# Optimization experiments

Hardware: AMD Instinct MI355X
Metric: run time of the kernel (lower is better)

The kernel has to match this reference:

```python
import jax, jax.numpy as jnp
import numpy as np

B, T, H = 32, 4096, 512


def setup_inputs() -> dict:
    key = jax.random.key(0)
    k1, k2, k3, k4, k5 = jax.random.split(key, 5)
    stdv = 1.0 / np.sqrt(2 * H)
    stdv_v = 1.0 / np.sqrt(H)
    return {
        "hidden": jax.random.normal(k1, (B, H), dtype=jnp.float32),
        "encoder_outputs": jax.random.normal(k2, (T, B, H), dtype=jnp.float32),
        "W_attn": jax.random.uniform(k3, (H, 2 * H), minval=-stdv, maxval=stdv, dtype=jnp.float32),
        "b_attn": jax.random.uniform(k4, (H,), minval=-stdv, maxval=stdv, dtype=jnp.float32),
        "v": jax.random.uniform(k5, (H,), minval=-stdv_v, maxval=stdv_v, dtype=jnp.float32),
    }


def reference(hidden, encoder_outputs, W_attn, b_attn, v):
    # hidden: [B, H]; encoder_outputs: [T, B, H]
    T_ = encoder_outputs.shape[0]
    h = jnp.broadcast_to(hidden[None, :, :], (T_,) + hidden.shape).transpose(1, 0, 2)  # [B,T,H]
    enc = encoder_outputs.transpose(1, 0, 2)  # [B,T,H]
    cat = jnp.concatenate([h, enc], axis=2)  # [B,T,2H]
    # Linear(2H -> H) then legacy F.softmax with implicit dim=0 for 3D input (batch axis)
    energy = jax.nn.softmax(jnp.einsum('btk,hk->bth', cat, W_attn) + b_attn, axis=0)  # [B,T,H]
    # bmm(v[B,1,H], energy^T[B,H,T]) -> [B,1,T] -> squeeze -> [B,T]
    scores = jnp.einsum('h,bth->bt', v, energy)
    return jax.nn.relu(scores)[:, None, :]  # [B,1,T]
```

## Files before the change

kernel.cpp:

```cpp
#include <hip/hip_runtime.h>
#include <hip/hip_bf16.h>

#define B_ 32
#define T_ 4096
#define H_ 512
#define TILE_T 4
#define M_TILE 128
#define BK 64
#define KSTEPS 8
#define NTHREADS 512

typedef __attribute__((ext_vector_type(8))) short short8;
typedef __attribute__((ext_vector_type(8))) __bf16 bf16x8;
typedef __attribute__((ext_vector_type(4))) float f32x4;

__device__ __forceinline__ short f2bf(float f) {
    unsigned u = __builtin_bit_cast(unsigned, f);
    u = (u + 0x7fffu + ((u >> 16) & 1u)) >> 16;
    return (short)u;
}

__global__ void prep_w2f(const float* __restrict__ W, short* __restrict__ w2f) {
    int idx = blockIdx.x * 256 + threadIdx.x;
    int j    = idx & 7;
    int lane = (idx >> 3) & 63;
    int ni   = (idx >> 9) & 3;
    int ks   = (idx >> 11) & 1;
    int kk   = (idx >> 12) & 7;
    int c    = (idx >> 15) & 7;
    int h = c * 64 + ni * 16 + (lane & 15);
    int k = kk * 64 + ks * 32 + (lane >> 4) * 8 + j;
    w2f[idx] = f2bf(W[h * (2 * H_) + H_ + k]);
}

__global__ void prep_hid(const float* __restrict__ hidden,
                         const float* __restrict__ W,
                         const float* __restrict__ bias,
                         float* __restrict__ hidproj) {
    __shared__ float hrow[H_];
    int b = blockIdx.y;
    int h = blockIdx.x * 128 + threadIdx.x;
    for (int i = threadIdx.x; i < H_; i += 128) hrow[i] = hidden[b * H_ + i];
    __syncthreads();
    const float* wr = W + (size_t)h * (2 * H_);
    float acc = bias[h];
#pragma unroll 4
    for (int k = 0; k < H_; k += 4) {
        acc += hrow[k]     * wr[k];
        acc += hrow[k + 1] * wr[k + 1];
        acc += hrow[k + 2] * wr[k + 2];
        acc += hrow[k + 3] * wr[k + 3];
    }
    hidproj[b * H_ + h] = acc;
}

__global__ __launch_bounds__(NTHREADS, 2)
void attn_main(const float* __restrict__ enc,
               const float* __restrict__ hidproj,
               const short* __restrict__ w2f,
               const float* __restrict__ vvec,
               float* __restrict__ out)
{
    __shared__ __align__(16) short lds_a[2][M_TILE * BK];

    const int tid  = threadIdx.x;
    const int lane = tid & 63;
    const int wid  = tid >> 6;
    const int t0   = blockIdx.x * TILE_T;
    const int n0   = wid * 64;
    const int lo   = lane & 15;
    const int hi4  = lane >> 4;

    f32x4 acc[8][4];
#pragma unroll
    for (int i = 0; i < 8; ++i)
#pragma unroll
        for (int j = 0; j < 4; ++j) acc[i][j] = f32x4{0.f, 0.f, 0.f, 0.f};

    const short* wbase = w2f + (size_t)wid * 32768 + lane * 8;

    const int arow = tid >> 2;
    const int akc  = tid & 3;
    const float* abase = enc + (size_t)(t0 * B_ + arow) * H_ + akc * 16;
    const int aw0 = arow * BK + (((2 * akc)     ^ (arow & 7)) << 3);
    const int aw1 = arow * BK + (((2 * akc + 1) ^ (arow & 7)) << 3);

    {
        f32x4 x0 = *(const f32x4*)(abase);
        f32x4 x1 = *(const f32x4*)(abase + 4);
        f32x4 x2 = *(const f32x4*)(abase + 8);
        f32x4 x3 = *(const f32x4*)(abase + 12);
        short8 p0, p1;
        p0[0]=f2bf(x0[0]); p0[1]=f2bf(x0[1]); p0[2]=f2bf(x0[2]); p0[3]=f2bf(x0[3]);
        p0[4]=f2bf(x1[0]); p0[5]=f2bf(x1[1]); p0[6]=f2bf(x1[2]); p0[7]=f2bf(x1[3]);
        p1[0]=f2bf(x2[0]); p1[1]=f2bf(x2[1]); p1[2]=f2bf(x2[2]); p1[3]=f2bf(x2[3]);
        p1[4]=f2bf(x3[0]); p1[5]=f2bf(x3[1]); p1[6]=f2bf(x3[2]); p1[7]=f2bf(x3[3]);
        *(short8*)&lds_a[0][aw0] = p0;
        *(short8*)&lds_a[0][aw1] = p1;
        asm volatile("s_waitcnt lgkmcnt(0)" ::: "memory");
        __builtin_amdgcn_s_barrier();
    }

    for (int kk = 0; kk < KSTEPS; ++kk) {
        const int cur = kk & 1;
        const bool pf = (kk + 1) < KSTEPS;
        const short* __restrict__ ab = &lds_a[cur][0];
        short* __restrict__ adst = &lds_a[cur ^ 1][0];

        bf16x8 b0[4], b1[4];
#pragma unroll
        for (int ni = 0; ni < 4; ++ni)
            b0[ni] = *(const bf16x8*)(wbase + ((kk * 2 + 0) * 4 + ni) * 512);
#pragma unroll
        for (int ni = 0; ni < 4; ++ni)
            b1[ni] = *(const bf16x8*)(wbase + ((kk * 2 + 1) * 4 + ni) * 512);

        f32x4 x0, x1, x2, x3;
        if (pf) {
            const float* asrc = abase + (size_t)(kk + 1) * BK;
            x0 = *(const f32x4*)(asrc);
            x1 = *(const f32x4*)(asrc + 4);
            x2 = *(const f32x4*)(asrc + 8);
            x3 = *(const f32x4*)(asrc + 12);
        }

        {
            bf16x8 af[4];
#pragma unroll
            for (int mi = 0; mi < 4; ++mi) {
                int r = mi * 16 + lo;
                af[mi] = *(const bf16x8*)&ab[r * BK + ((hi4 ^ (r & 7)) << 3)];
            }
            __builtin_amdgcn_s_setprio(1);
#pragma unroll
            for (int mi = 0; mi < 4; ++mi)
#pragma unroll
                for (int ni = 0; ni < 4; ++ni)
                    acc[mi][ni] = __builtin_amdgcn_mfma_f32_16x16x32_bf16(
                        af[mi], b0[ni], acc[mi][ni], 0, 0, 0);
            __builtin_amdgcn_s_setprio(0);
#pragma unroll
            for (int mi = 0; mi < 4; ++mi) {
                int r = (mi + 4) * 16 + lo;
                af[mi] = *(const bf16x8*)&ab[r * BK + ((hi4 ^ (r & 7)) << 3)];
            }
            __builtin_amdgcn_s_setprio(1);
#pragma unroll
            for (int mi = 0; mi < 4; ++mi)
#pragma unroll
                for (int ni = 0; ni < 4; ++ni)
                    acc[mi + 4][ni] = __builtin_amdgcn_mfma_f32_16x16x32_bf16(
                        af[mi], b0[ni], acc[mi + 4][ni], 0, 0, 0);
            __builtin_amdgcn_s_setprio(0);
        }

        if (pf) {
            short8 p0;
            p0[0]=f2bf(x0[0]); p0[1]=f2bf(x0[1]); p0[2]=f2bf(x0[2]); p0[3]=f2bf(x0[3]);
            p0[4]=f2bf(x1[0]); p0[5]=f2bf(x1[1]); p0[6]=f2bf(x1[2]); p0[7]=f2bf(x1[3]);
            *(short8*)&adst[aw0] = p0;
        }

        {
            bf16x8 af[4];
#pragma unroll
            for (int mi = 0; mi < 4; ++mi) {
                int r = mi * 16 + lo;
                af[mi] = *(const bf16x8*)&ab[r * BK + (((4 | hi4) ^ (r & 7)) << 3)];
            }
            __builtin_amdgcn_s_setprio(1);
#pragma unroll
            for (int mi = 0; mi < 4; ++mi)
#pragma unroll
                for (int ni = 0; ni < 4; ++ni)
                    acc[mi][ni] = __builtin_amdgcn_mfma_f32_16x16x32_bf16(
                        af[mi], b1[ni], acc[mi][ni], 0, 0, 0);
            __builtin_amdgcn_s_setprio(0);
#pragma unroll
            for (int mi = 0; mi < 4; ++mi) {
                int r = (mi + 4) * 16 + lo;
                af[mi] = *(const bf16x8*)&ab[r * BK + (((4 | hi4) ^ (r & 7)) << 3)];
            }
            __builtin_amdgcn_s_setprio(1);
#pragma unroll
            for (int mi = 0; mi < 4; ++mi)
#pragma unroll
                for (int ni = 0; ni < 4; ++ni)
                    acc[mi + 4][ni] = __builtin_amdgcn_mfma_f32_16x16x32_bf16(
                        af[mi], b1[ni], acc[mi + 4][ni], 0, 0, 0);
            __builtin_amdgcn_s_setprio(0);
        }

        if (pf) {
            short8 p1;
            p1[0]=f2bf(x2[0]); p1[1]=f2bf(x2[1]); p1[2]=f2bf(x2[2]); p1[3]=f2bf(x2[3]);
            p1[4]=f2bf(x3[0]); p1[5]=f2bf(x3[1]); p1[6]=f2bf(x3[2]); p1[7]=f2bf(x3[3]);
            *(short8*)&adst[aw1] = p1;
        }

        asm volatile("s_waitcnt lgkmcnt(0)" ::: "memory");
        __builtin_amdgcn_s_barrier();
    }

    {
        float hp[2][4][4];
#pragma unroll
        for (int par = 0; par < 2; ++par)
#pragma unroll
            for (int j = 0; j < 4; ++j) {
                int b = par * 16 + hi4 * 4 + j;
#pragma unroll
                for (int ni = 0; ni < 4; ++ni)
                    hp[par][j][ni] = hidproj[b * H_ + n0 + ni * 16 + lo];
            }
#pragma unroll
        for (int mi = 0; mi < 8; ++mi)
#pragma unroll
            for (int ni = 0; ni < 4; ++ni)
#pragma unroll
                for (int j = 0; j < 4; ++j)
                    acc[mi][ni][j] += hp[mi & 1][j][ni];
    }

    float vh[4];
#pragma unroll
    for (int ni = 0; ni < 4; ++ni) vh[ni] = vvec[n0 + ni * 16 + lo];

    float scp[8][4];
#pragma unroll
    for (int tl = 0; tl < 4; ++tl) {
        const int m0 = tl * 2, m1 = tl * 2 + 1;
#pragma unroll
        for (int ni = 0; ni < 4; ++ni) {
            float mx = -1e30f;
#pragma unroll
            for (int j = 0; j < 4; ++j) {
                mx = fmaxf(mx, acc[m0][ni][j]);
                mx = fmaxf(mx, acc[m1][ni][j]);
            }
            mx = fmaxf(mx, __shfl_xor(mx, 16));
            mx = fmaxf(mx, __shfl_xor(mx, 32));
            float e0[4], e1[4];
            float sum = 0.f;
#pragma unroll
            for (int j = 0; j < 4; ++j) {
                e0[j] = __expf(acc[m0][ni][j] - mx);
                e1[j] = __expf(acc[m1][ni][j] - mx);
                sum += e0[j] + e1[j];
            }
            sum += __shfl_xor(sum, 16);
            sum += __shfl_xor(sum, 32);
            float rs = vh[ni] / sum;
#pragma unroll
            for (int j = 0; j < 4; ++j) {
                if (ni == 0) { scp[m0][j] = e0[j] * rs; scp[m1][j] = e1[j] * rs; }
                else         { scp[m0][j] += e0[j] * rs; scp[m1][j] += e1[j] * rs; }
            }
        }
    }

#pragma unroll
    for (int mi = 0; mi < 8; ++mi)
#pragma unroll
        for (int j = 0; j < 4; ++j) {
            float x = scp[mi][j];
            x += __shfl_xor(x, 1);
            x += __shfl_xor(x, 2);
            x += __shfl_xor(x, 4);
            x += __shfl_xor(x, 8);
            scp[mi][j] = x;
        }

    __syncthreads();
    float* red = (float*)&lds_a[0][0];
    if (lo == 0) {
#pragma unroll
        for (int mi = 0; mi < 8; ++mi)
#pragma unroll
            for (int j = 0; j < 4; ++j)
                red[wid * 128 + mi * 16 + hi4 * 4 + j] = scp[mi][j];
    }
    __syncthreads();
    if (tid < 128) {
        float s = 0.f;
#pragma unroll
        for (int w = 0; w < 8; ++w) s += red[w * 128 + tid];
        int b  = tid & 31;
        int tl = tid >> 5;
        out[(size_t)b * T_ + (t0 + tl)] = fmaxf(s, 0.f);
    }
}

extern "C" void kernel_launch(void* const* d_in, const int* in_sizes, int n_in,
                              void* d_out, int out_size, void* d_ws, size_t ws_size,
                              hipStream_t stream) {
    const float* hidden = (const float*)d_in[0];
    const float* enc    = (const float*)d_in[1];
    const float* W      = (const float*)d_in[2];
    const float* bias   = (const float*)d_in[3];
    const float* v      = (const float*)d_in[4];
    float* out = (float*)d_out;

    float* hidproj = (float*)d_ws;
    short* w2f     = (short*)((char*)d_ws + 65536);

    prep_w2f<<<1024, 256, 0, stream>>>(W, w2f);
    prep_hid<<<dim3(4, 32), 128, 0, stream>>>(hidden, W, bias, hidproj);
    attn_main<<<T_ / TILE_T, NTHREADS, 0, stream>>>(enc, hidproj, w2f, v, out);
}
```

Measured before the change: 128.6 us.

## Split the H dimension across two workgroups and reduce partial scores in a finish kernel

Each workgroup now has 256 threads and covers half of the 512 output columns, so the grid doubles to 2048 blocks. Block indices are swizzled so that the two halves of the same time tile run next to each other and can share enc reads in L2. Each half writes partial scores to workspace, and a new finish kernel adds the halves and applies ReLU. The aim is more parallelism and occupancy, at the cost of staging the A tile twice (twice the fp32 load and convert work per output) and an extra kernel launch.

```diff
diff --git a/kernel.cpp b/kernel.cpp
--- a/kernel.cpp
+++ b/kernel.cpp
@@ -8,7 +8,7 @@
 #define M_TILE 128
 #define BK 64
 #define KSTEPS 8
-#define NTHREADS 512
+#define NTHREADS 256
 
 typedef __attribute__((ext_vector_type(8))) short short8;
 typedef __attribute__((ext_vector_type(8))) __bf16 bf16x8;
@@ -54,22 +54,30 @@
     hidproj[b * H_ + h] = acc;
 }
 
+__global__ void finish(const float* __restrict__ sp, float* __restrict__ out) {
+    int i = blockIdx.x * 256 + threadIdx.x;
+    out[i] = fmaxf(sp[i] + sp[131072 + i], 0.f);
+}
+
 __global__ __launch_bounds__(NTHREADS, 2)
 void attn_main(const float* __restrict__ enc,
                const float* __restrict__ hidproj,
                const short* __restrict__ w2f,
                const float* __restrict__ vvec,
-               float* __restrict__ out)
+               float* __restrict__ spart)
 {
     __shared__ __align__(16) short lds_a[2][M_TILE * BK];
 
     const int tid  = threadIdx.x;
     const int lane = tid & 63;
     const int wid  = tid >> 6;
-    const int t0   = blockIdx.x * TILE_T;
-    const int n0   = wid * 64;
+    const int bid  = blockIdx.x;
+    const int tau  = ((bid >> 4) << 3) | (bid & 7);
+    const int eta  = (bid >> 3) & 1;
+    const int t0   = tau * TILE_T;
     const int lo   = lane & 15;
     const int hi4  = lane >> 4;
+    const int cblk = eta * 4 + wid;
 
     f32x4 acc[8][4];
 #pragma unroll
@@ -77,26 +85,35 @@
 #pragma unroll
         for (int j = 0; j < 4; ++j) acc[i][j] = f32x4{0.f, 0.f, 0.f, 0.f};
 
-    const short* wbase = w2f + (size_t)wid * 32768 + lane * 8;
-
-    const int arow = tid >> 2;
-    const int akc  = tid & 3;
-    const float* abase = enc + (size_t)(t0 * B_ + arow) * H_ + akc * 16;
-    const int aw0 = arow * BK + (((2 * akc)     ^ (arow & 7)) << 3);
-    const int aw1 = arow * BK + (((2 * akc + 1) ^ (arow & 7)) << 3);
+    const short* wbase = w2f + (size_t)cblk * 32768 + lane * 8;
+
+    const int arow = tid >> 1;
+    const int ah   = tid & 1;
+    const float* abase = enc + (size_t)(t0 * B_ + arow) * H_ + ah * 32;
+    const int aw0 = arow * BK + (((4 * ah + 0) ^ (arow & 7)) << 3);
+    const int aw1 = arow * BK + (((4 * ah + 1) ^ (arow & 7)) << 3);
+    const int aw2 = arow * BK + (((4 * ah + 2) ^ (arow & 7)) << 3);
+    const int aw3 = arow * BK + (((4 * ah + 3) ^ (arow & 7)) << 3);
+
+#define CVT2(P, XA, XB)                                                         \
+    P[0]=f2bf(XA[0]); P[1]=f2bf(XA[1]); P[2]=f2bf(XA[2]); P[3]=f2bf(XA[3]);     \
+    P[4]=f2bf(XB[0]); P[5]=f2bf(XB[1]); P[6]=f2bf(XB[2]); P[7]=f2bf(XB[3]);
 
     {
         f32x4 x0 = *(const f32x4*)(abase);
         f32x4 x1 = *(const f32x4*)(abase + 4);
         f32x4 x2 = *(const f32x4*)(abase + 8);
         f32x4 x3 = *(const f32x4*)(abase + 12);
-        short8 p0, p1;
-        p0[0]=f2bf(x0[0]); p0[1]=f2bf(x0[1]); p0[2]=f2bf(x0[2]); p0[3]=f2bf(x0[3]);
-        p0[4]=f2bf(x1[0]); p0[5]=f2bf(x1[1]); p0[6]=f2bf(x1[2]); p0[7]=f2bf(x1[3]);
-        p1[0]=f2bf(x2[0]); p1[1]=f2bf(x2[1]); p1[2]=f2bf(x2[2]); p1[3]=f2bf(x2[3]);
-        p1[4]=f2bf(x3[0]); p1[5]=f2bf(x3[1]); p1[6]=f2bf(x3[2]); p1[7]=f2bf(x3[3]);
+        f32x4 x4 = *(const f32x4*)(abase + 16);
+        f32x4 x5 = *(const f32x4*)(abase + 20);
+        f32x4 x6 = *(const f32x4*)(abase + 24);
+        f32x4 x7 = *(const f32x4*)(abase + 28);
+        short8 p0, p1, p2, p3;
+        CVT2(p0, x0, x1) CVT2(p1, x2, x3) CVT2(p2, x4, x5) CVT2(p3, x6, x7)
         *(short8*)&lds_a[0][aw0] = p0;
         *(short8*)&lds_a[0][aw1] = p1;
+        *(short8*)&lds_a[0][aw2] = p2;
+        *(short8*)&lds_a[0][aw3] = p3;
         asm volatile("s_waitcnt lgkmcnt(0)" ::: "memory");
         __builtin_amdgcn_s_barrier();
     }
@@ -115,13 +132,13 @@
         for (int ni = 0; ni < 4; ++ni)
             b1[ni] = *(const bf16x8*)(wbase + ((kk * 2 + 1) * 4 + ni) * 512);
 
-        f32x4 x0, x1, x2, x3;
+        f32x4 x0, x1, x2, x3, x4, x5, x6, x7;
         if (pf) {
             const float* asrc = abase + (size_t)(kk + 1) * BK;
-            x0 = *(const f32x4*)(asrc);
-            x1 = *(const f32x4*)(asrc + 4);
-            x2 = *(const f32x4*)(asrc + 8);
-            x3 = *(const f32x4*)(asrc + 12);
+            x0 = *(const f32x4*)(asrc);      x1 = *(const f32x4*)(asrc + 4);
+            x2 = *(const f32x4*)(asrc + 8);  x3 = *(const f32x4*)(asrc + 12);
+            x4 = *(const f32x4*)(asrc + 16); x5 = *(const f32x4*)(asrc + 20);
+            x6 = *(const f32x4*)(asrc + 24); x7 = *(const f32x4*)(asrc + 28);
         }
 
         {
@@ -155,10 +172,10 @@
         }
 
         if (pf) {
-            short8 p0;
-            p0[0]=f2bf(x0[0]); p0[1]=f2bf(x0[1]); p0[2]=f2bf(x0[2]); p0[3]=f2bf(x0[3]);
-            p0[4]=f2bf(x1[0]); p0[5]=f2bf(x1[1]); p0[6]=f2bf(x1[2]); p0[7]=f2bf(x1[3]);
+            short8 p0, p1;
+            CVT2(p0, x0, x1) CVT2(p1, x2, x3)
             *(short8*)&adst[aw0] = p0;
+            *(short8*)&adst[aw1] = p1;
         }
 
         {
@@ -192,15 +209,16 @@
         }
 
         if (pf) {
-            short8 p1;
-            p1[0]=f2bf(x2[0]); p1[1]=f2bf(x2[1]); p1[2]=f2bf(x2[2]); p1[3]=f2bf(x2[3]);
-            p1[4]=f2bf(x3[0]); p1[5]=f2bf(x3[1]); p1[6]=f2bf(x3[2]); p1[7]=f2bf(x3[3]);
-            *(short8*)&adst[aw1] = p1;
+            short8 p2, p3;
+            CVT2(p2, x4, x5) CVT2(p3, x6, x7)
+            *(short8*)&adst[aw2] = p2;
+            *(short8*)&adst[aw3] = p3;
         }
 
         asm volatile("s_waitcnt lgkmcnt(0)" ::: "memory");
         __builtin_amdgcn_s_barrier();
     }
+#undef CVT2
 
     {
         float hp[2][4][4];
@@ -211,7 +229,7 @@
                 int b = par * 16 + hi4 * 4 + j;
 #pragma unroll
                 for (int ni = 0; ni < 4; ++ni)
-                    hp[par][j][ni] = hidproj[b * H_ + n0 + ni * 16 + lo];
+                    hp[par][j][ni] = hidproj[b * H_ + cblk * 64 + ni * 16 + lo];
             }
 #pragma unroll
         for (int mi = 0; mi < 8; ++mi)
@@ -224,7 +242,7 @@
 
     float vh[4];
 #pragma unroll
-    for (int ni = 0; ni < 4; ++ni) vh[ni] = vvec[n0 + ni * 16 + lo];
+    for (int ni = 0; ni < 4; ++ni) vh[ni] = vvec[cblk * 64 + ni * 16 + lo];
 
     float scp[8][4];
 #pragma unroll
@@ -282,12 +300,10 @@
     }
     __syncthreads();
     if (tid < 128) {
-        float s = 0.f;
-#pragma unroll
-        for (int w = 0; w < 8; ++w) s += red[w * 128 + tid];
+        float s = red[tid] + red[128 + tid] + red[256 + tid] + red[384 + tid];
         int b  = tid & 31;
         int tl = tid >> 5;
-        out[(size_t)b * T_ + (t0 + tl)] = fmaxf(s, 0.f);
+        spart[(size_t)eta * 131072 + (size_t)b * T_ + (t0 + tl)] = s;
     }
 }
 
@@ -303,8 +319,10 @@
 
     float* hidproj = (float*)d_ws;
     short* w2f     = (short*)((char*)d_ws + 65536);
+    float* spart   = (float*)((char*)d_ws + 65536 + 524288);
 
     prep_w2f<<<1024, 256, 0, stream>>>(W, w2f);
     prep_hid<<<dim3(4, 32), 128, 0, stream>>>(hidden, W, bias, hidproj);
-    attn_main<<<T_ / TILE_T, NTHREADS, 0, stream>>>(enc, hidproj, w2f, v, out);
-}
+    attn_main<<<2048, NTHREADS, 0, stream>>>(enc, hidproj, w2f, v, spart);
+    finish<<<512, 256, 0, stream>>>(spart, out);
+}
```

New measurement: 140.4 us. 1.09x slower.
